# Optimization experiments

Hardware: AMD Instinct MI355X
Metric: run time of the kernel (lower is better)

## Reference

```python
import jax, jax.numpy as jnp
import numpy as np

DIM = 1024
HEADS = 16


def setup_inputs() -> dict:
    key = jax.random.key(0)
    k1, k2, k3, k4 = jax.random.split(key, 4)
    x = jax.random.normal(k1, (4, 2048, DIM), dtype=jnp.float32)
    # torch nn.Linear weights: [out_features, in_features]
    w_qkv = jax.random.normal(k2, (3 * DIM, DIM), dtype=jnp.float32) * (DIM ** -0.5)
    w_out = jax.random.normal(k3, (DIM, DIM), dtype=jnp.float32) * (DIM ** -0.5)
    b_out = jax.random.normal(k4, (DIM,), dtype=jnp.float32) * 0.01
    return {"x": x, "w_qkv": w_qkv, "w_out": w_out, "b_out": b_out}


def reference(x, w_qkv, w_out, b_out):
    b, n, d = x.shape
    h = HEADS
    hd = d // h
    scale = d ** -0.5  # note: full dim, matching the original module
    qkv = jnp.einsum('bnd,ed->bne', x, w_qkv)  # [b, n, 3d]
    q, k, v = jnp.split(qkv, 3, axis=-1)
    def to_heads(t):
        return t.reshape(b, n, h, hd).transpose(0, 2, 1, 3)  # [b, h, n, hd]
    q, k, v = map(to_heads, (q, k, v))
    dots = jnp.einsum('bhqd,bhkd->bhqk', q, k) * scale  # [b, h, n, n]
    attn = jax.nn.softmax(dots, axis=-1)
    out = jnp.einsum('bhqk,bhkd->bhqd', attn, v)  # [b, h, n, hd]
    out = out.transpose(0, 2, 1, 3).reshape(b, n, d)
    return jnp.einsum('bnd,ed->bne', out, w_out) + b_out
```

## Files before the change

kernel.cpp:

```cpp
#include <hip/hip_runtime.h>
#include <stdint.h>

#define SEQ   2048
#define NDIM  1024
#define NH    16
#define HD    64
#define KDIM  1024

typedef short  short8  __attribute__((ext_vector_type(8)));
typedef float  floatx4 __attribute__((ext_vector_type(4)));
typedef float  floatx16 __attribute__((ext_vector_type(16)));
typedef unsigned short ushort4v __attribute__((ext_vector_type(4)));
typedef _Float16 half8 __attribute__((ext_vector_type(8)));
typedef __fp16  fp16x2 __attribute__((ext_vector_type(2)));
typedef unsigned int uint2v __attribute__((ext_vector_type(2)));
typedef unsigned int uint4v __attribute__((ext_vector_type(4)));

typedef __attribute__((address_space(1))) void GV;
typedef __attribute__((address_space(3))) void LV;

#define QSCALE 0.04508422003f

__device__ __forceinline__ unsigned short f2bf(float f) {
    unsigned int u = __float_as_uint(f);
    u += 0x7fffu + ((u >> 16) & 1u);
    return (unsigned short)(u >> 16);
}

__device__ __forceinline__ float ex2(float x) {
#if __has_builtin(__builtin_amdgcn_exp2f)
    return __builtin_amdgcn_exp2f(x);
#else
    return exp2f(x);
#endif
}

__device__ __forceinline__ void pl32swap(unsigned int &a, unsigned int &b) {
#if __has_builtin(__builtin_amdgcn_permlane32_swap)
    uint2v r = __builtin_amdgcn_permlane32_swap(a, b, false, false);
    a = r.x; b = r.y;
#else
    asm("v_permlane32_swap_b32 %0, %1" : "+v"(a), "+v"(b));
#endif
}

__global__ __launch_bounds__(256) void cast_f32_bf16(const float* __restrict__ in,
                                                     unsigned short* __restrict__ out) {
    int i = (blockIdx.x * 256 + threadIdx.x) * 4;
    float4 v = *(const float4*)(in + i);
    ushort4v o;
    o.x = f2bf(v.x); o.y = f2bf(v.y); o.z = f2bf(v.z); o.w = f2bf(v.w);
    *(ushort4v*)(out + i) = o;
}

template<int MODE>
__global__ __launch_bounds__(256, 3)
void gemm_bt(const unsigned short* __restrict__ A,
             const unsigned short* __restrict__ B,
             unsigned short* __restrict__ Cq,
             unsigned short* __restrict__ Ck,
             unsigned short* __restrict__ Cv,
             const float* __restrict__ bias,
             float* __restrict__ Cout)
{
    __shared__ unsigned short As[2][4096];
    __shared__ unsigned short Bs[2][4096];
    const int tid  = threadIdx.x;
    const int lane = tid & 63;
    const int w    = tid >> 6;
    const int quad = lane >> 4;
    const int l15  = lane & 15;
    const int wm   = w >> 1, wn = w & 1;
    const int bm   = blockIdx.x, bn = blockIdx.y;

    const unsigned short* Arow = A + (size_t)bm * 128 * KDIM;
    const unsigned short* Brow = B + (size_t)bn * 128 * KDIM;

    const unsigned short* ga[2]; const unsigned short* gb[2];
    unsigned short* la[2][2];    unsigned short* lb[2][2];
#pragma unroll
    for (int i = 0; i < 2; ++i) {
        int j = ((w * 2 + i) << 6) + lane;
        int r = j >> 2;
        int c = (j & 3) ^ ((r >> 1) & 3);
        ga[i] = Arow + r * KDIM + c * 8;
        gb[i] = Brow + r * KDIM + c * 8;
#pragma unroll
        for (int b = 0; b < 2; ++b) {
            la[b][i] = &As[b][(w * 2 + i) << 9];
            lb[b][i] = &Bs[b][(w * 2 + i) << 9];
        }
    }

    int achunk[4], bchunk[4];
#pragma unroll
    for (int t = 0; t < 4; ++t) {
        int ra = wm * 64 + t * 16 + l15;
        achunk[t] = (ra << 2) + (quad ^ ((ra >> 1) & 3));
        int rb = wn * 64 + t * 16 + l15;
        bchunk[t] = (rb << 2) + (quad ^ ((rb >> 1) & 3));
    }

    floatx4 acc[4][4];
#pragma unroll
    for (int mt = 0; mt < 4; ++mt)
#pragma unroll
        for (int nt = 0; nt < 4; ++nt)
            acc[mt][nt] = (floatx4){0.f, 0.f, 0.f, 0.f};

#pragma unroll
    for (int i = 0; i < 2; ++i) {
        __builtin_amdgcn_global_load_lds((GV*)(void*)ga[i], (LV*)(void*)la[0][i], 16, 0, 0);
        __builtin_amdgcn_global_load_lds((GV*)(void*)gb[i], (LV*)(void*)lb[0][i], 16, 0, 0);
    }

    for (int kt = 0; kt < KDIM / 32; ++kt) {
        const int buf = kt & 1;
        __syncthreads();
        if (kt < KDIM / 32 - 1) {
#pragma unroll
            for (int i = 0; i < 2; ++i) {
                __builtin_amdgcn_global_load_lds((GV*)(void*)(ga[i] + (kt + 1) * 32), (LV*)(void*)la[buf ^ 1][i], 16, 0, 0);
                __builtin_amdgcn_global_load_lds((GV*)(void*)(gb[i] + (kt + 1) * 32), (LV*)(void*)lb[buf ^ 1][i], 16, 0, 0);
            }
        }
        short8 af[4], bf[4];
#pragma unroll
        for (int t = 0; t < 4; ++t) {
            af[t] = *(const short8*)(&As[buf][0] + (achunk[t] << 3));
            bf[t] = *(const short8*)(&Bs[buf][0] + (bchunk[t] << 3));
        }
#pragma unroll
        for (int mt = 0; mt < 4; ++mt)
#pragma unroll
            for (int nt = 0; nt < 4; ++nt)
                acc[mt][nt] = __builtin_amdgcn_mfma_f32_16x16x32_bf16(af[mt], bf[nt], acc[mt][nt], 0, 0, 0);
    }

    if (MODE == 0) {
        const int which = bn >> 3;
        unsigned short* dst = which == 0 ? Cq : (which == 1 ? Ck : Cv);
        if (which == 2) {
#pragma unroll
            for (int nt = 0; nt < 4; ++nt) {
                int e0   = ((bn & 7) << 7) + wn * 64 + nt * 16;
                int head = e0 >> 6;
                int hd   = (e0 & 63) + l15;
#pragma unroll
                for (int mt = 0; mt < 4; ++mt) {
                    int n0 = bm * 128 + wm * 64 + mt * 16 + quad * 4;
                    int b  = n0 >> 11;
                    int n  = n0 & 2047;
                    int bh = (b << 4) + head;
                    size_t base = (size_t)bh * 131072
                                + (size_t)(n >> 6) * 4096
                                + (size_t)((((hd >> 5) << 2) + ((n >> 4) & 3)) << 9)
                                + ((((n >> 3) & 1) << 5) + (hd & 31)) * 8
                                + (n & 7);
                    fp16x2 p01 = __builtin_amdgcn_cvt_pkrtz(acc[mt][nt][0], acc[mt][nt][1]);
                    fp16x2 p23 = __builtin_amdgcn_cvt_pkrtz(acc[mt][nt][2], acc[mt][nt][3]);
                    uint2v st;
                    st.x = __builtin_bit_cast(unsigned int, p01);
                    st.y = __builtin_bit_cast(unsigned int, p23);
                    *(uint2v*)(dst + base) = st;
                }
            }
        } else {
#pragma unroll
            for (int nt = 0; nt < 4; ++nt) {
                int e0   = ((bn & 7) << 7) + wn * 64 + nt * 16;
                int head = e0 >> 6;
                int hd   = (e0 & 63) + l15;
#pragma unroll
                for (int mt = 0; mt < 4; ++mt) {
#pragma unroll
                    for (int r = 0; r < 4; ++r) {
                        int m = bm * 128 + wm * 64 + mt * 16 + quad * 4 + r;
                        int b = m >> 11, n = m & 2047;
                        int bh = (b << 4) + head;
                        float val = acc[mt][nt][r];
                        if (which == 0) {
                            dst[((size_t)bh * SEQ + n) * HD + hd] = f2bf(val * QSCALE);
                        } else {
                            size_t idx = (size_t)bh * 131072
                                       + (size_t)(n >> 6) * 4096
                                       + (size_t)(((((n >> 5) & 1) << 2) + (hd >> 4)) << 9)
                                       + ((((hd >> 3) & 1) << 5) + (n & 31)) * 8
                                       + (hd & 7);
                            dst[idx] = f2bf(val);
                        }
                    }
                }
            }
        }
    } else {
#pragma unroll
        for (int nt = 0; nt < 4; ++nt) {
            int e = bn * 128 + wn * 64 + nt * 16 + l15;
            float bv = bias[e];
#pragma unroll
            for (int mt = 0; mt < 4; ++mt) {
#pragma unroll
                for (int r = 0; r < 4; ++r) {
                    int m = bm * 128 + wm * 64 + mt * 16 + quad * 4 + r;
                    Cout[(size_t)m * NDIM + e] = acc[mt][nt][r] + bv;
                }
            }
        }
    }
}

__global__ __launch_bounds__(256, 4)
void attn_fused(const unsigned short* __restrict__ qb,
                const unsigned short* __restrict__ kfrag,
                const unsigned short* __restrict__ vfrag,
                unsigned short* __restrict__ ob)
{
    __shared__ unsigned short Ks[2][4096];
    __shared__ unsigned short Vs[2][4096];

    const int tid  = threadIdx.x;
    const int lane = tid & 63;
    const int w    = tid >> 6;
    const int l31  = lane & 31;
    const int half = lane >> 5;

    const int bid  = blockIdx.x;
    const int xcd  = bid & 7;
    const int slot = bid >> 3;
    const int bh   = xcd * 8 + (slot >> 4);
    const int q0   = (slot & 15) * 128;

    const unsigned short* Qb = qb    + (size_t)bh * SEQ * HD;
    const unsigned short* Kb = kfrag + (size_t)bh * 131072;
    const unsigned short* Vb = vfrag + (size_t)bh * 131072;

    short8 qf[4];
    {
        const unsigned short* qrow = Qb + (size_t)(q0 + w * 32 + l31) * HD + half * 8;
#pragma unroll
        for (int ks = 0; ks < 4; ++ks)
            qf[ks] = *(const short8*)(qrow + ks * 16);
    }

    floatx16 oacc[2];
#pragma unroll
    for (int ht = 0; ht < 2; ++ht)
#pragma unroll
        for (int i = 0; i < 16; ++i) oacc[ht][i] = 0.f;
    float lp0 = 0.f, lp1 = 0.f, lp2 = 0.f, lp3 = 0.f;

    const unsigned short* gk[2]; const unsigned short* gv[2];
    unsigned short* lk[2][2];    unsigned short* lv[2][2];
#pragma unroll
    for (int i = 0; i < 2; ++i) {
        int off = (((w * 2 + i) << 6) + lane) * 8;
        gk[i] = Kb + off;
        gv[i] = Vb + off;
#pragma unroll
        for (int b = 0; b < 2; ++b) {
            lk[b][i] = &Ks[b][(w * 2 + i) << 9];
            lv[b][i] = &Vs[b][(w * 2 + i) << 9];
        }
    }

#pragma unroll
    for (int i = 0; i < 2; ++i) {
        __builtin_amdgcn_global_load_lds((GV*)(void*)gk[i], (LV*)(void*)lk[0][i], 16, 0, 0);
        __builtin_amdgcn_global_load_lds((GV*)(void*)gv[i], (LV*)(void*)lv[0][i], 16, 0, 0);
    }

    for (int t = 0; t < 32; ++t) {
        const int buf = t & 1;
        __syncthreads();
        if (t < 31) {
#pragma unroll
            for (int i = 0; i < 2; ++i) {
                __builtin_amdgcn_global_load_lds((GV*)(void*)(gk[i] + (t + 1) * 4096), (LV*)(void*)lk[buf ^ 1][i], 16, 0, 0);
                __builtin_amdgcn_global_load_lds((GV*)(void*)(gv[i] + (t + 1) * 4096), (LV*)(void*)lv[buf ^ 1][i], 16, 0, 0);
            }
        }
        const unsigned short* KsB = Ks[buf];
        const unsigned short* VsB = Vs[buf];

#pragma unroll
        for (int kt = 0; kt < 2; ++kt) {
            floatx16 s;
#pragma unroll
            for (int i = 0; i < 16; ++i) s[i] = 0.f;
            __builtin_amdgcn_s_setprio(1);
#pragma unroll
            for (int ks = 0; ks < 4; ++ks) {
                short8 kf = *(const short8*)(KsB + ((kt * 4 + ks) << 9) + lane * 8);
                s = __builtin_amdgcn_mfma_f32_32x32x16_bf16(kf, qf[ks], s, 0, 0, 0);
            }
            __builtin_amdgcn_s_setprio(0);

            float e[16];
#pragma unroll
            for (int i = 0; i < 16; ++i) e[i] = ex2(s[i]);
            lp0 += (e[0] + e[1]) + (e[2] + e[3]);
            lp1 += (e[4] + e[5]) + (e[6] + e[7]);
            lp2 += (e[8] + e[9]) + (e[10] + e[11]);
            lp3 += (e[12] + e[13]) + (e[14] + e[15]);
            unsigned int u[8];
#pragma unroll
            for (int j = 0; j < 8; ++j) {
                fp16x2 p = __builtin_amdgcn_cvt_pkrtz(e[2 * j], e[2 * j + 1]);
                u[j] = __builtin_bit_cast(unsigned int, p);
            }
            pl32swap(u[0], u[2]); pl32swap(u[1], u[3]);
            pl32swap(u[4], u[6]); pl32swap(u[5], u[7]);
            half8 pb0, pb1;
            { uint4v t0; t0.x = u[0]; t0.y = u[1]; t0.z = u[2]; t0.w = u[3];
              pb0 = __builtin_bit_cast(half8, t0); }
            { uint4v t1; t1.x = u[4]; t1.y = u[5]; t1.z = u[6]; t1.w = u[7];
              pb1 = __builtin_bit_cast(half8, t1); }

            __builtin_amdgcn_s_setprio(1);
#pragma unroll
            for (int ht = 0; ht < 2; ++ht) {
                uint4v v0 = *(const uint4v*)(VsB + (((ht << 2) + kt * 2) << 9) + lane * 8);
                uint4v v1 = *(const uint4v*)(VsB + (((ht << 2) + kt * 2 + 1) << 9) + lane * 8);
                oacc[ht] = __builtin_amdgcn_mfma_f32_32x32x16_f16(__builtin_bit_cast(half8, v0), pb0, oacc[ht], 0, 0, 0);
                oacc[ht] = __builtin_amdgcn_mfma_f32_32x32x16_f16(__builtin_bit_cast(half8, v1), pb1, oacc[ht], 0, 0, 0);
            }
            __builtin_amdgcn_s_setprio(0);
        }
    }

    float lfull = (lp0 + lp1) + (lp2 + lp3);
    lfull += __shfl_xor(lfull, 32);
    float inv = 1.f / lfull;
    const int b = bh >> 4, h = bh & 15;
    const int qg = q0 + w * 32 + l31;
    unsigned short* orow = ob + ((size_t)b * SEQ + qg) * NDIM + h * HD;
#pragma unroll
    for (int ht = 0; ht < 2; ++ht) {
#pragma unroll
        for (int g = 0; g < 4; ++g) {
            int hd0 = ht * 32 + g * 8 + half * 4;
            unsigned int w0 = (unsigned int)f2bf(oacc[ht][g * 4 + 0] * inv)
                            | ((unsigned int)f2bf(oacc[ht][g * 4 + 1] * inv) << 16);
            unsigned int w1 = (unsigned int)f2bf(oacc[ht][g * 4 + 2] * inv)
                            | ((unsigned int)f2bf(oacc[ht][g * 4 + 3] * inv) << 16);
            uint2v st; st.x = w0; st.y = w1;
            *(uint2v*)(orow + hd0) = st;
        }
    }
}

extern "C" void kernel_launch(void* const* d_in, const int* in_sizes, int n_in,
                              void* d_out, int out_size, void* d_ws, size_t ws_size,
                              hipStream_t stream)
{
    (void)in_sizes; (void)n_in; (void)out_size; (void)ws_size;
    const float* x    = (const float*)d_in[0];
    const float* wqkv = (const float*)d_in[1];
    const float* wout = (const float*)d_in[2];
    const float* bout = (const float*)d_in[3];
    float* out = (float*)d_out;

    unsigned short* xb    = (unsigned short*)d_ws;
    unsigned short* wqkvb = xb    + 8388608;
    unsigned short* woutb = wqkvb + 3145728;
    unsigned short* qbuf  = woutb + 1048576;
    unsigned short* kbuf  = qbuf  + 8388608;
    unsigned short* vbuf  = kbuf  + 8388608;
    unsigned short* obuf  = vbuf  + 8388608;

    cast_f32_bf16<<<8192, 256, 0, stream>>>(x, xb);
    cast_f32_bf16<<<3072, 256, 0, stream>>>(wqkv, wqkvb);
    cast_f32_bf16<<<1024, 256, 0, stream>>>(wout, woutb);

    gemm_bt<0><<<dim3(64, 24), 256, 0, stream>>>(xb, wqkvb, qbuf, kbuf, vbuf, nullptr, nullptr);
    attn_fused<<<1024, 256, 0, stream>>>(qbuf, kbuf, vbuf, obuf);
    gemm_bt<1><<<dim3(64, 8), 256, 0, stream>>>(obuf, woutb, nullptr, nullptr, nullptr, bout, out);
}
```

Before: 274.2 us.

## Process two 32-row query tiles per wave to reuse K/V LDS loads

Each wave now handles 64 query rows (two 32-row tiles), so every K and V fragment read from shared memory feeds two MFMAs. The attention grid is halved to 512 blocks of 256 queries each, and the launch bound drops to 2 blocks per CU to leave room for the extra registers. The softmax row-sum is now accumulated with fdot2 on the packed fp16 probabilities, which also changes rounding slightly. In exchange, register pressure rises and fewer blocks are resident to hide latency.

```diff
diff --git a/kernel.cpp b/kernel.cpp
--- a/kernel.cpp
+++ b/kernel.cpp
@@ -210,7 +210,7 @@
     }
 }
 
-__global__ __launch_bounds__(256, 4)
+__global__ __launch_bounds__(256, 2)
 void attn_fused(const unsigned short* __restrict__ qb,
                 const unsigned short* __restrict__ kfrag,
                 const unsigned short* __restrict__ vfrag,
@@ -228,27 +228,30 @@
     const int bid  = blockIdx.x;
     const int xcd  = bid & 7;
     const int slot = bid >> 3;
-    const int bh   = xcd * 8 + (slot >> 4);
-    const int q0   = (slot & 15) * 128;
+    const int bh   = xcd * 8 + (slot >> 3);
+    const int q0   = (slot & 7) * 256;
 
     const unsigned short* Qb = qb    + (size_t)bh * SEQ * HD;
     const unsigned short* Kb = kfrag + (size_t)bh * 131072;
     const unsigned short* Vb = vfrag + (size_t)bh * 131072;
 
-    short8 qf[4];
+    short8 qfA[4], qfB[4];
     {
-        const unsigned short* qrow = Qb + (size_t)(q0 + w * 32 + l31) * HD + half * 8;
-#pragma unroll
-        for (int ks = 0; ks < 4; ++ks)
-            qf[ks] = *(const short8*)(qrow + ks * 16);
-    }
-
-    floatx16 oacc[2];
+        const unsigned short* qrowA = Qb + (size_t)(q0 + w * 64 + l31) * HD + half * 8;
+        const unsigned short* qrowB = qrowA + 32 * HD;
+#pragma unroll
+        for (int ks = 0; ks < 4; ++ks) {
+            qfA[ks] = *(const short8*)(qrowA + ks * 16);
+            qfB[ks] = *(const short8*)(qrowB + ks * 16);
+        }
+    }
+
+    floatx16 oaccA[2], oaccB[2];
 #pragma unroll
     for (int ht = 0; ht < 2; ++ht)
 #pragma unroll
-        for (int i = 0; i < 16; ++i) oacc[ht][i] = 0.f;
-    float lp0 = 0.f, lp1 = 0.f, lp2 = 0.f, lp3 = 0.f;
+        for (int i = 0; i < 16; ++i) { oaccA[ht][i] = 0.f; oaccB[ht][i] = 0.f; }
+    float lA = 0.f, lB = 0.f;
 
     const unsigned short* gk[2]; const unsigned short* gv[2];
     unsigned short* lk[2][2];    unsigned short* lv[2][2];
@@ -285,67 +288,88 @@
 
 #pragma unroll
         for (int kt = 0; kt < 2; ++kt) {
-            floatx16 s;
-#pragma unroll
-            for (int i = 0; i < 16; ++i) s[i] = 0.f;
+            floatx16 sA, sB;
+#pragma unroll
+            for (int i = 0; i < 16; ++i) { sA[i] = 0.f; sB[i] = 0.f; }
             __builtin_amdgcn_s_setprio(1);
 #pragma unroll
             for (int ks = 0; ks < 4; ++ks) {
                 short8 kf = *(const short8*)(KsB + ((kt * 4 + ks) << 9) + lane * 8);
-                s = __builtin_amdgcn_mfma_f32_32x32x16_bf16(kf, qf[ks], s, 0, 0, 0);
+                sA = __builtin_amdgcn_mfma_f32_32x32x16_bf16(kf, qfA[ks], sA, 0, 0, 0);
+                sB = __builtin_amdgcn_mfma_f32_32x32x16_bf16(kf, qfB[ks], sB, 0, 0, 0);
             }
             __builtin_amdgcn_s_setprio(0);
 
-            float e[16];
-#pragma unroll
-            for (int i = 0; i < 16; ++i) e[i] = ex2(s[i]);
-            lp0 += (e[0] + e[1]) + (e[2] + e[3]);
-            lp1 += (e[4] + e[5]) + (e[6] + e[7]);
-            lp2 += (e[8] + e[9]) + (e[10] + e[11]);
-            lp3 += (e[12] + e[13]) + (e[14] + e[15]);
-            unsigned int u[8];
-#pragma unroll
-            for (int j = 0; j < 8; ++j) {
-                fp16x2 p = __builtin_amdgcn_cvt_pkrtz(e[2 * j], e[2 * j + 1]);
-                u[j] = __builtin_bit_cast(unsigned int, p);
-            }
-            pl32swap(u[0], u[2]); pl32swap(u[1], u[3]);
-            pl32swap(u[4], u[6]); pl32swap(u[5], u[7]);
-            half8 pb0, pb1;
-            { uint4v t0; t0.x = u[0]; t0.y = u[1]; t0.z = u[2]; t0.w = u[3];
-              pb0 = __builtin_bit_cast(half8, t0); }
-            { uint4v t1; t1.x = u[4]; t1.y = u[5]; t1.z = u[6]; t1.w = u[7];
-              pb1 = __builtin_bit_cast(half8, t1); }
+            half8 pA0, pA1, pB0, pB1;
+            {
+                fp16x2 ones; ones[0] = (__fp16)1.0f; ones[1] = (__fp16)1.0f;
+                unsigned int ua[8], ub[8];
+#pragma unroll
+                for (int j = 0; j < 8; ++j) {
+                    fp16x2 pa = __builtin_amdgcn_cvt_pkrtz(ex2(sA[2 * j]), ex2(sA[2 * j + 1]));
+                    fp16x2 pb = __builtin_amdgcn_cvt_pkrtz(ex2(sB[2 * j]), ex2(sB[2 * j + 1]));
+                    ua[j] = __builtin_bit_cast(unsigned int, pa);
+                    ub[j] = __builtin_bit_cast(unsigned int, pb);
+#if __has_builtin(__builtin_amdgcn_fdot2)
+                    lA = __builtin_amdgcn_fdot2(pa, ones, lA, false);
+                    lB = __builtin_amdgcn_fdot2(pb, ones, lB, false);
+#else
+                    lA += (float)pa[0] + (float)pa[1];
+                    lB += (float)pb[0] + (float)pb[1];
+#endif
+                }
+                pl32swap(ua[0], ua[2]); pl32swap(ua[1], ua[3]);
+                pl32swap(ua[4], ua[6]); pl32swap(ua[5], ua[7]);
+                pl32swap(ub[0], ub[2]); pl32swap(ub[1], ub[3]);
+                pl32swap(ub[4], ub[6]); pl32swap(ub[5], ub[7]);
+                uint4v t0, t1, t2, t3;
+                t0.x = ua[0]; t0.y = ua[1]; t0.z = ua[2]; t0.w = ua[3];
+                t1.x = ua[4]; t1.y = ua[5]; t1.z = ua[6]; t1.w = ua[7];
+                t2.x = ub[0]; t2.y = ub[1]; t2.z = ub[2]; t2.w = ub[3];
+                t3.x = ub[4]; t3.y = ub[5]; t3.z = ub[6]; t3.w = ub[7];
+                pA0 = __builtin_bit_cast(half8, t0);
+                pA1 = __builtin_bit_cast(half8, t1);
+                pB0 = __builtin_bit_cast(half8, t2);
+                pB1 = __builtin_bit_cast(half8, t3);
+            }
 
             __builtin_amdgcn_s_setprio(1);
 #pragma unroll
             for (int ht = 0; ht < 2; ++ht) {
                 uint4v v0 = *(const uint4v*)(VsB + (((ht << 2) + kt * 2) << 9) + lane * 8);
                 uint4v v1 = *(const uint4v*)(VsB + (((ht << 2) + kt * 2 + 1) << 9) + lane * 8);
-                oacc[ht] = __builtin_amdgcn_mfma_f32_32x32x16_f16(__builtin_bit_cast(half8, v0), pb0, oacc[ht], 0, 0, 0);
-                oacc[ht] = __builtin_amdgcn_mfma_f32_32x32x16_f16(__builtin_bit_cast(half8, v1), pb1, oacc[ht], 0, 0, 0);
+                half8 vf0 = __builtin_bit_cast(half8, v0);
+                half8 vf1 = __builtin_bit_cast(half8, v1);
+                oaccA[ht] = __builtin_amdgcn_mfma_f32_32x32x16_f16(vf0, pA0, oaccA[ht], 0, 0, 0);
+                oaccB[ht] = __builtin_amdgcn_mfma_f32_32x32x16_f16(vf0, pB0, oaccB[ht], 0, 0, 0);
+                oaccA[ht] = __builtin_amdgcn_mfma_f32_32x32x16_f16(vf1, pA1, oaccA[ht], 0, 0, 0);
+                oaccB[ht] = __builtin_amdgcn_mfma_f32_32x32x16_f16(vf1, pB1, oaccB[ht], 0, 0, 0);
             }
             __builtin_amdgcn_s_setprio(0);
         }
     }
 
-    float lfull = (lp0 + lp1) + (lp2 + lp3);
-    lfull += __shfl_xor(lfull, 32);
-    float inv = 1.f / lfull;
     const int b = bh >> 4, h = bh & 15;
-    const int qg = q0 + w * 32 + l31;
-    unsigned short* orow = ob + ((size_t)b * SEQ + qg) * NDIM + h * HD;
-#pragma unroll
-    for (int ht = 0; ht < 2; ++ht) {
-#pragma unroll
-        for (int g = 0; g < 4; ++g) {
-            int hd0 = ht * 32 + g * 8 + half * 4;
-            unsigned int w0 = (unsigned int)f2bf(oacc[ht][g * 4 + 0] * inv)
-                            | ((unsigned int)f2bf(oacc[ht][g * 4 + 1] * inv) << 16);
-            unsigned int w1 = (unsigned int)f2bf(oacc[ht][g * 4 + 2] * inv)
-                            | ((unsigned int)f2bf(oacc[ht][g * 4 + 3] * inv) << 16);
-            uint2v st; st.x = w0; st.y = w1;
-            *(uint2v*)(orow + hd0) = st;
+#pragma unroll
+    for (int tile = 0; tile < 2; ++tile) {
+        float lfull = tile == 0 ? lA : lB;
+        lfull += __shfl_xor(lfull, 32);
+        float inv = 1.f / lfull;
+        const floatx16* oc = tile == 0 ? oaccA : oaccB;
+        const int qg = q0 + w * 64 + tile * 32 + l31;
+        unsigned short* orow = ob + ((size_t)b * SEQ + qg) * NDIM + h * HD;
+#pragma unroll
+        for (int ht = 0; ht < 2; ++ht) {
+#pragma unroll
+            for (int g = 0; g < 4; ++g) {
+                int hd0 = ht * 32 + g * 8 + half * 4;
+                unsigned int w0 = (unsigned int)f2bf(oc[ht][g * 4 + 0] * inv)
+                                | ((unsigned int)f2bf(oc[ht][g * 4 + 1] * inv) << 16);
+                unsigned int w1 = (unsigned int)f2bf(oc[ht][g * 4 + 2] * inv)
+                                | ((unsigned int)f2bf(oc[ht][g * 4 + 3] * inv) << 16);
+                uint2v st; st.x = w0; st.y = w1;
+                *(uint2v*)(orow + hd0) = st;
+            }
         }
     }
 }
@@ -374,6 +398,6 @@
     cast_f32_bf16<<<1024, 256, 0, stream>>>(wout, woutb);
 
     gemm_bt<0><<<dim3(64, 24), 256, 0, stream>>>(xb, wqkvb, qbuf, kbuf, vbuf, nullptr, nullptr);
-    attn_fused<<<1024, 256, 0, stream>>>(qbuf, kbuf, vbuf, obuf);
+    attn_fused<<<512, 256, 0, stream>>>(qbuf, kbuf, vbuf, obuf);
     gemm_bt<1><<<dim3(64, 8), 256, 0, stream>>>(obuf, woutb, nullptr, nullptr, nullptr, bout, out);
 }
```

After: 257.3 us. -6.2%, faster.
